# Kernel tuning notes

Measured on AMD Instinct MI355X. Metric: run time of the kernel, lower is better.

Reference implementation:

```python
import jax, jax.numpy as jnp
import numpy as np

H = 16            # num heads (sharded)
NOPE = 128        # qk_nope_head_dim
ROPE = 64         # qk_rope_head_dim
VD = 128          # v_head_dim
KV_RANK = 512
HEAD = NOPE + ROPE  # 192
SCALE = HEAD ** (-0.5)  # mscale == 1 (no yarn scaling)
EPS = 1e-6


def rmsnorm(x, w):
    var = jnp.mean(x * x, axis=-1, keepdims=True)
    return x * jax.lax.rsqrt(var + EPS) * w


def apply_rope(pe, cos, sin):
    # pe: [T, h, ROPE]; torch code de-interleaves pairs then applies
    # non-interleaved (rotate-half) rope: out = [e*cos - o*sin, o*cos + e*sin]
    e = pe[..., 0::2]
    o = pe[..., 1::2]
    c = cos[:, None, :]
    s = sin[:, None, :]
    return jnp.concatenate([e * c - o * s, o * c + e * s], axis=-1)


def setup_inputs() -> dict:
    key = jax.random.key(0)
    ks = jax.random.split(key, 10)
    T, D = 4096, 2048
    w = 0.02
    return {
        "hidden_states": jax.random.normal(ks[0], (T, D), jnp.float32),
        "cos": jax.random.uniform(ks[1], (T, ROPE // 2), jnp.float32),
        "sin": jax.random.uniform(ks[2], (T, ROPE // 2), jnp.float32),
        "w_q_a": jax.random.normal(ks[3], (D, 1536), jnp.float32) * w,
        "q_a_ln_w": jnp.ones((1536,), jnp.float32),
        "w_q_b": jax.random.normal(ks[4], (1536, H * HEAD), jnp.float32) * w,
        "w_kv_a": jax.random.normal(ks[5], (D, KV_RANK + ROPE), jnp.float32) * w,
        "kv_a_ln_w": jnp.ones((KV_RANK,), jnp.float32),
        "w_kv_b": jax.random.normal(ks[6], (KV_RANK, H * (NOPE + VD)), jnp.float32) * w,
        "w_o": jax.random.normal(ks[7], (H * VD, D), jnp.float32) * w,
        "batch_size": 2,
    }


def reference(hidden_states, cos, sin, w_q_a, q_a_ln_w, w_q_b, w_kv_a,
              kv_a_ln_w, w_kv_b, w_o, batch_size):
    T, D = hidden_states.shape
    B = int(batch_size)
    S = T // B

    # Q: low-rank down proj -> RMSNorm -> up proj
    q = rmsnorm(hidden_states @ w_q_a, q_a_ln_w) @ w_q_b
    q = q.reshape(T, H, HEAD)
    q_nope = q[..., :NOPE]
    q_pe = apply_rope(q[..., NOPE:], cos, sin)

    # KV: joint down proj with shared rope part (MQA-style)
    ckv = hidden_states @ w_kv_a                        # [T, 512+64]
    compressed_kv = ckv[:, :KV_RANK]
    k_pe = apply_rope(ckv[:, KV_RANK:][:, None, :], cos, sin)  # [T, 1, 64]
    kv = (rmsnorm(compressed_kv, kv_a_ln_w) @ w_kv_b).reshape(T, H, NOPE + VD)
    k_nope = kv[..., :NOPE]
    v = kv[..., NOPE:]                                   # [T, H, 128]

    # Assemble full query/key heads (value pad to 192 + final slice is a no-op
    # mathematically since padded dims are zero; we keep value dim = 128).
    query = jnp.concatenate([q_nope, q_pe], axis=-1)     # [T, H, 192]
    key = jnp.concatenate([k_nope, jnp.broadcast_to(k_pe, (T, H, ROPE))], axis=-1)

    # Causal (prefill) attention per sequence
    qb = query.reshape(B, S, H, HEAD)
    kb = key.reshape(B, S, H, HEAD)
    vb = v.reshape(B, S, H, VD)
    scores = jnp.einsum("bqhd,bkhd->bhqk", qb, kb) * SCALE
    causal = jnp.tril(jnp.ones((S, S), bool))
    scores = jnp.where(causal, scores, jnp.finfo(scores.dtype).min)
    probs = jax.nn.softmax(scores, axis=-1)
    attn = jnp.einsum("bhqk,bkhd->bqhd", probs, vb)      # [B, S, H, 128]

    return attn.reshape(T, H * VD) @ w_o
```

## Files before the change

kernel.cpp:

```cpp
#include <hip/hip_runtime.h>
#include <cstdint>
#include <cstddef>

#define TT 4096
#define DD 2048
#define NH 16
#define HEADD 192
#define NOPE 128
#define VDIM 128
#define SEQ 2048

typedef __bf16 bf16x8 __attribute__((ext_vector_type(8)));
typedef float f32x4 __attribute__((ext_vector_type(4)));
typedef unsigned int u32;

__device__ __forceinline__ float bf2f(unsigned short u) {
    union { unsigned int i; float f; } v; v.i = ((unsigned int)u) << 16; return v.f;
}
__device__ __forceinline__ unsigned short f2bf(float f) {
    union { float f; unsigned int i; } v; v.f = f;
    unsigned int r = v.i + 0x7FFFu + ((v.i >> 16) & 1u);
    return (unsigned short)(r >> 16);
}
__device__ __forceinline__ u32 pack2bf(float a, float b) {
    return (u32)f2bf(a) | ((u32)f2bf(b) << 16);
}
__device__ __forceinline__ void gload16(const unsigned short* g, unsigned short* l) {
    __builtin_amdgcn_global_load_lds((const __attribute__((address_space(1))) u32*)g,
                                     (__attribute__((address_space(3))) u32*)l, 16, 0, 0);
}

__global__ __launch_bounds__(256) void cvt_bf16_k(const float* __restrict__ x,
                                                  unsigned short* __restrict__ y, int n) {
    int i = (blockIdx.x * 256 + threadIdx.x) * 4;
    if (i < n) {
        float4 v = *(const float4*)(x + i);
        uint2 o;
        o.x = pack2bf(v.x, v.y);
        o.y = pack2bf(v.z, v.w);
        *(uint2*)(y + i) = o;
    }
}

__global__ __launch_bounds__(256) void transpose_cvt_k(const float* __restrict__ W,
                                                       unsigned short* __restrict__ Wt,
                                                       int K, int N) {
    __shared__ float tile[32][33];
    int n0 = blockIdx.x * 32, k0 = blockIdx.y * 32;
    int t = threadIdx.x, lr = t >> 5, lc = t & 31;
#pragma unroll
    for (int p = 0; p < 4; p++) {
        int k = k0 + lr + p * 8, n = n0 + lc;
        tile[lr + p * 8][lc] = (k < K && n < N) ? W[(size_t)k * N + n] : 0.f;
    }
    __syncthreads();
#pragma unroll
    for (int p = 0; p < 4; p++) {
        int n = n0 + lr + p * 8, k = k0 + lc;
        if (n < N && k < K) Wt[(size_t)n * K + k] = f2bf(tile[lc][lr + p * 8]);
    }
}

__global__ __launch_bounds__(256) void gemm_bf16_k(const unsigned short* __restrict__ A,
                                                   const unsigned short* __restrict__ Bt,
                                                   float* __restrict__ C,
                                                   int M, int N, int K) {
    __shared__ __align__(16) unsigned short As[128 * 32];
    __shared__ __align__(16) unsigned short Bs[128 * 32];
    int bm = blockIdx.y * 128, bn = blockIdx.x * 128;
    int t = threadIdx.x;
    int wave = t >> 6, lane = t & 63;
    int wr = (wave >> 1) * 64, wc = (wave & 1) * 64;
    int l15 = lane & 15, quad = lane >> 4;
    f32x4 acc[4][4];
    f32x4 zero = {0.f, 0.f, 0.f, 0.f};
#pragma unroll
    for (int i = 0; i < 4; i++)
#pragma unroll
        for (int j = 0; j < 4; j++) acc[i][j] = zero;
    int r0 = 16 * (2 * wave) + (lane >> 2);
    int cOff = (lane & 3) * 8;
    const unsigned short* gA0 = A + (size_t)(bm + r0) * K + cOff;
    const unsigned short* gA1 = A + (size_t)(bm + r0 + 16) * K + cOff;
    const unsigned short* gB0 = Bt + (size_t)(bn + r0) * K + cOff;
    const unsigned short* gB1 = Bt + (size_t)(bn + r0 + 16) * K + cOff;
    unsigned short* lA0 = &As[(2 * wave) * 512];
    unsigned short* lA1 = &As[(2 * wave + 1) * 512];
    unsigned short* lB0 = &Bs[(2 * wave) * 512];
    unsigned short* lB1 = &Bs[(2 * wave + 1) * 512];
    for (int k0 = 0; k0 < K; k0 += 32) {
        gload16(gA0 + k0, lA0);
        gload16(gA1 + k0, lA1);
        gload16(gB0 + k0, lB0);
        gload16(gB1 + k0, lB1);
        __syncthreads();
        bf16x8 af[4], bfr[4];
#pragma unroll
        for (int i = 0; i < 4; i++)
            af[i] = *(const bf16x8*)&As[(wr + i * 16 + l15) * 32 + quad * 8];
#pragma unroll
        for (int j = 0; j < 4; j++)
            bfr[j] = *(const bf16x8*)&Bs[(wc + j * 16 + l15) * 32 + quad * 8];
#pragma unroll
        for (int i = 0; i < 4; i++)
#pragma unroll
            for (int j = 0; j < 4; j++)
                acc[i][j] = __builtin_amdgcn_mfma_f32_16x16x32_bf16(af[i], bfr[j], acc[i][j], 0, 0, 0);
        __syncthreads();
    }
#pragma unroll
    for (int i = 0; i < 4; i++) {
        int row = bm + wr + i * 16 + quad * 4;
#pragma unroll
        for (int j = 0; j < 4; j++) {
            int col = bn + wc + j * 16 + l15;
            if (col < N) {
                float* cp = C + (size_t)row * N + col;
#pragma unroll
                for (int r = 0; r < 4; r++) cp[(size_t)r * N] = acc[i][j][r];
            }
        }
    }
}

__global__ __launch_bounds__(256) void gemm_bf16o_k(const unsigned short* __restrict__ A,
                                                    const unsigned short* __restrict__ Bt,
                                                    unsigned short* __restrict__ C,
                                                    int M, int N, int K) {
    __shared__ __align__(16) unsigned short As[128 * 32];
    __shared__ __align__(16) unsigned short Bs[128 * 32];
    int bm = blockIdx.y * 128, bn = blockIdx.x * 128;
    int t = threadIdx.x;
    int wave = t >> 6, lane = t & 63;
    int wr = (wave >> 1) * 64, wc = (wave & 1) * 64;
    int l15 = lane & 15, quad = lane >> 4;
    f32x4 acc[4][4];
    f32x4 zero = {0.f, 0.f, 0.f, 0.f};
#pragma unroll
    for (int i = 0; i < 4; i++)
#pragma unroll
        for (int j = 0; j < 4; j++) acc[i][j] = zero;
    int r0 = 16 * (2 * wave) + (lane >> 2);
    int cOff = (lane & 3) * 8;
    const unsigned short* gA0 = A + (size_t)(bm + r0) * K + cOff;
    const unsigned short* gA1 = A + (size_t)(bm + r0 + 16) * K + cOff;
    const unsigned short* gB0 = Bt + (size_t)(bn + r0) * K + cOff;
    const unsigned short* gB1 = Bt + (size_t)(bn + r0 + 16) * K + cOff;
    unsigned short* lA0 = &As[(2 * wave) * 512];
    unsigned short* lA1 = &As[(2 * wave + 1) * 512];
    unsigned short* lB0 = &Bs[(2 * wave) * 512];
    unsigned short* lB1 = &Bs[(2 * wave + 1) * 512];
    for (int k0 = 0; k0 < K; k0 += 32) {
        gload16(gA0 + k0, lA0);
        gload16(gA1 + k0, lA1);
        gload16(gB0 + k0, lB0);
        gload16(gB1 + k0, lB1);
        __syncthreads();
        bf16x8 af[4], bfr[4];
#pragma unroll
        for (int i = 0; i < 4; i++)
            af[i] = *(const bf16x8*)&As[(wr + i * 16 + l15) * 32 + quad * 8];
#pragma unroll
        for (int j = 0; j < 4; j++)
            bfr[j] = *(const bf16x8*)&Bs[(wc + j * 16 + l15) * 32 + quad * 8];
#pragma unroll
        for (int i = 0; i < 4; i++)
#pragma unroll
            for (int j = 0; j < 4; j++)
                acc[i][j] = __builtin_amdgcn_mfma_f32_16x16x32_bf16(af[i], bfr[j], acc[i][j], 0, 0, 0);
        __syncthreads();
    }
#pragma unroll
    for (int i = 0; i < 4; i++) {
        int row = bm + wr + i * 16 + quad * 4;
#pragma unroll
        for (int j = 0; j < 4; j++) {
            int col = bn + wc + j * 16 + l15;
            if (col < N) {
                unsigned short* cp = C + (size_t)row * N + col;
#pragma unroll
                for (int r = 0; r < 4; r++) cp[(size_t)r * N] = f2bf(acc[i][j][r]);
            }
        }
    }
}

#define KS_STRIDE 200
#define VT_STRIDE 72
#define CS_STRIDE 132

__global__ __launch_bounds__(256) void gemm_kv_k(const unsigned short* __restrict__ A,
                                                 const unsigned short* __restrict__ Bt,
                                                 unsigned short* __restrict__ Kb2,
                                                 unsigned short* __restrict__ Vt2) {
    const int K = 512;
    __shared__ __align__(16) unsigned short smem[128 * CS_STRIDE];
    unsigned short* As = smem;
    unsigned short* Bs = smem + 128 * 32;
    unsigned short* Cs = smem;
    int bm = blockIdx.y * 128, bn = blockIdx.x * 128;
    int t = threadIdx.x;
    int wave = t >> 6, lane = t & 63;
    int wr = (wave >> 1) * 64, wc = (wave & 1) * 64;
    int l15 = lane & 15, quad = lane >> 4;
    f32x4 acc[4][4];
    f32x4 zero = {0.f, 0.f, 0.f, 0.f};
#pragma unroll
    for (int i = 0; i < 4; i++)
#pragma unroll
        for (int j = 0; j < 4; j++) acc[i][j] = zero;
    int r0 = 16 * (2 * wave) + (lane >> 2);
    int cOff = (lane & 3) * 8;
    const unsigned short* gA0 = A + (size_t)(bm + r0) * K + cOff;
    const unsigned short* gA1 = A + (size_t)(bm + r0 + 16) * K + cOff;
    const unsigned short* gB0 = Bt + (size_t)(bn + r0) * K + cOff;
    const unsigned short* gB1 = Bt + (size_t)(bn + r0 + 16) * K + cOff;
    unsigned short* lA0 = &As[(2 * wave) * 512];
    unsigned short* lA1 = &As[(2 * wave + 1) * 512];
    unsigned short* lB0 = &Bs[(2 * wave) * 512];
    unsigned short* lB1 = &Bs[(2 * wave + 1) * 512];
    for (int k0 = 0; k0 < K; k0 += 32) {
        gload16(gA0 + k0, lA0);
        gload16(gA1 + k0, lA1);
        gload16(gB0 + k0, lB0);
        gload16(gB1 + k0, lB1);
        __syncthreads();
        bf16x8 af[4], bfr[4];
#pragma unroll
        for (int i = 0; i < 4; i++)
            af[i] = *(const bf16x8*)&As[(wr + i * 16 + l15) * 32 + quad * 8];
#pragma unroll
        for (int j = 0; j < 4; j++)
            bfr[j] = *(const bf16x8*)&Bs[(wc + j * 16 + l15) * 32 + quad * 8];
#pragma unroll
        for (int i = 0; i < 4; i++)
#pragma unroll
            for (int j = 0; j < 4; j++)
                acc[i][j] = __builtin_amdgcn_mfma_f32_16x16x32_bf16(af[i], bfr[j], acc[i][j], 0, 0, 0);
        __syncthreads();
    }
#pragma unroll
    for (int i = 0; i < 4; i++) {
        int lr = wr + i * 16 + quad * 4;
#pragma unroll
        for (int j = 0; j < 4; j++) {
            int lc = wc + j * 16 + l15;
#pragma unroll
            for (int r = 0; r < 4; r++)
                Cs[(lr + r) * CS_STRIDE + lc] = f2bf(acc[i][j][r]);
        }
    }
    __syncthreads();
    int hh = bn >> 8;
    bool isV = (bn & 255) != 0;
    if (!isV) {
        int row = t >> 1, halfc = t & 1;
        int gs = bm + row;
        int b2 = gs >> 11, s2 = gs & 2047;
        unsigned short* dp = Kb2 +
            ((size_t)((b2 * NH + hh) * 32 + (s2 >> 6)) * 64 + (s2 & 63)) * KS_STRIDE + halfc * 64;
        const unsigned short* sp = &Cs[row * CS_STRIDE + halfc * 64];
#pragma unroll
        for (int g = 0; g < 8; g++)
            *(uint4*)(dp + g * 8) = *(const uint4*)(sp + g * 8);
    } else {
        int kth = t >> 7, dim = t & 127;
        int gs0 = bm + kth * 64;
        int b2 = gs0 >> 11, s20 = gs0 & 2047;
        unsigned short* dp = Vt2 +
            ((size_t)((b2 * NH + hh) * 32 + (s20 >> 6)) * 128 + dim) * VT_STRIDE;
#pragma unroll
        for (int g = 0; g < 8; g++) {
            uint4 o;
            unsigned short* op = (unsigned short*)&o;
#pragma unroll
            for (int q2 = 0; q2 < 8; q2++)
                op[q2] = Cs[(kth * 64 + g * 8 + q2) * CS_STRIDE + dim];
            *(uint4*)(dp + g * 8) = o;
        }
    }
}

__global__ __launch_bounds__(256) void kpe_fill_k(const unsigned short* __restrict__ kpe,
                                                  unsigned short* __restrict__ Kb2) {
    int trow = blockIdx.x, t = threadIdx.x;
    int b = trow >> 11, s = trow & 2047;
    int kt = s >> 6, sr = s & 63;
    const unsigned short* src = kpe + trow * 64;
#pragma unroll
    for (int i = t; i < NH * 64; i += 256) {
        int h = i >> 6, d = i & 63;
        Kb2[(((size_t)(b * NH + h) * 32 + kt) * 64 + sr) * KS_STRIDE + 128 + d] = src[d];
    }
}

__global__ __launch_bounds__(256) void rmsnorm_bf_k(const unsigned short* __restrict__ x,
                                                    const float* __restrict__ w,
                                                    unsigned short* __restrict__ y) {
    int row = blockIdx.x, t = threadIdx.x;
    const unsigned short* xr = x + (size_t)row * 2112;
    float s = 0.f;
    for (int i = t; i < 1536; i += 256) { float v = bf2f(xr[i]); s += v * v; }
    __shared__ float red[256];
    red[t] = s; __syncthreads();
    for (int o = 128; o > 0; o >>= 1) { if (t < o) red[t] += red[t + o]; __syncthreads(); }
    float scale = rsqrtf(red[0] / 1536.f + 1e-6f);
    unsigned short* yr = y + (size_t)row * 1536;
    for (int i = t; i < 1536; i += 256) yr[i] = f2bf(bf2f(xr[i]) * scale * w[i]);
}

__global__ __launch_bounds__(256) void kvprep_bf_k(const unsigned short* __restrict__ qab,
                                                   const float* __restrict__ w,
                                                   const float* __restrict__ cosb,
                                                   const float* __restrict__ sinb,
                                                   unsigned short* __restrict__ ckvn,
                                                   unsigned short* __restrict__ kpe) {
    int row = blockIdx.x, t = threadIdx.x;
    const unsigned short* xr = qab + (size_t)row * 2112 + 1536;
    float s = 0.f;
#pragma unroll
    for (int i = t; i < 512; i += 256) { float v = bf2f(xr[i]); s += v * v; }
    __shared__ float red[256];
    red[t] = s; __syncthreads();
    for (int o = 128; o > 0; o >>= 1) { if (t < o) red[t] += red[t + o]; __syncthreads(); }
    float scale = rsqrtf(red[0] / 512.f + 1e-6f);
    unsigned short* yr = ckvn + (size_t)row * 512;
#pragma unroll
    for (int i = t; i < 512; i += 256) yr[i] = f2bf(bf2f(xr[i]) * scale * w[i]);
    if (t < 32) {
        float e = bf2f(xr[512 + 2 * t]), o = bf2f(xr[512 + 2 * t + 1]);
        float c = cosb[row * 32 + t], sn = sinb[row * 32 + t];
        kpe[row * 64 + t]      = f2bf(e * c - o * sn);
        kpe[row * 64 + 32 + t] = f2bf(o * c + e * sn);
    }
}

__global__ __launch_bounds__(256) void qprep_bf_k(const unsigned short* __restrict__ q,
                                                  const float* __restrict__ cosb,
                                                  const float* __restrict__ sinb,
                                                  unsigned short* __restrict__ Qb) {
    const float SCALE = 0.07216878364870323f;
    int trow = blockIdx.x, t = threadIdx.x;
    const unsigned short* qr = q + (size_t)trow * (NH * HEADD);
    unsigned short* yr = Qb + (size_t)trow * (NH * HEADD);
    for (int i = t; i < NH * HEADD; i += 256) {
        int h = i / HEADD, d = i - h * HEADD;
        float val;
        if (d < NOPE) val = bf2f(qr[i]);
        else {
            int j = d - NOPE;
            int jj = j & 31;
            const unsigned short* pe = qr + h * HEADD + NOPE;
            float e = bf2f(pe[2 * jj]), o = bf2f(pe[2 * jj + 1]);
            float c = cosb[trow * 32 + jj], sn = sinb[trow * 32 + jj];
            val = (j < 32) ? (e * c - o * sn) : (o * c + e * sn);
        }
        yr[i] = f2bf(val * SCALE);
    }
}

__global__ __launch_bounds__(512) void attn_mfma_k(const unsigned short* __restrict__ Qb,
                                                   const unsigned short* __restrict__ Kb2,
                                                   const unsigned short* __restrict__ Vt2,
                                                   unsigned short* __restrict__ Opart,
                                                   float* __restrict__ Mbuf,
                                                   float* __restrict__ Lbuf) {
    __shared__ __align__(16) unsigned short Ks[64 * KS_STRIDE];
    __shared__ __align__(16) unsigned short Vts[128 * VT_STRIDE];
    int xe = 39 - blockIdx.x;
    int h  = blockIdx.y;
    int b  = blockIdx.z;
    int qt = 0, accn = 0;
    while (true) { int c = (qt >> 2) + 1; if (xe < accn + c) break; accn += c; qt++; }
    int chunk = xe - accn;
    int t = threadIdx.x;
    int w = t >> 6, lane = t & 63;
    int l15 = lane & 15, quad = lane >> 4;
    int bh = b * NH + h;
    int q0 = b * SEQ + qt * 128;
    int qglob = qt * 128 + w * 16 + l15;
    int flat = bh * 40 + xe;

    bf16x8 qf[6];
    {
        const unsigned short* qbase = Qb + ((size_t)(q0 + w * 16 + l15) * NH + h) * HEADD + quad * 8;
#pragma unroll
        for (int c = 0; c < 6; c++)
            qf[c] = *(const bf16x8*)(qbase + c * 32);
    }
    f32x4 acc_o[8];
    f32x4 zero = {0.f, 0.f, 0.f, 0.f};
#pragma unroll
    for (int j = 0; j < 8; j++) acc_o[j] = zero;
    float mrun = -1e30f, lrun = 0.f;

    int kt0 = chunk * 8, kt1 = min(kt0 + 7, 2 * qt + 1);
    int cbeg = w * 5 + min(w, 3), cnt = (w < 3) ? 6 : 5;
    for (int kt = kt0; kt <= kt1; kt++) {
        __syncthreads();
        {
            const unsigned short* kg = Kb2 + ((size_t)bh * 32 + kt) * (64 * KS_STRIDE) + lane * 8;
            const unsigned short* vg = Vt2 + ((size_t)bh * 32 + kt) * (128 * VT_STRIDE) + lane * 8;
            for (int c = cbeg; c < cbeg + cnt; c++) {
                if (c < 25) gload16(kg + c * 512, &Ks[c * 512]);
                else        gload16(vg + (c - 25) * 512, &Vts[(c - 25) * 512]);
            }
        }
        __syncthreads();
        f32x4 acc_s[4];
#pragma unroll
        for (int j = 0; j < 4; j++) acc_s[j] = zero;
#pragma unroll
        for (int c = 0; c < 6; c++) {
#pragma unroll
            for (int j = 0; j < 4; j++) {
                bf16x8 kf = *(const bf16x8*)&Ks[(j * 16 + l15) * KS_STRIDE + c * 32 + quad * 8];
                acc_s[j] = __builtin_amdgcn_mfma_f32_16x16x32_bf16(kf, qf[c], acc_s[j], 0, 0, 0);
            }
        }
        float sv[4][4];
        const bool needmask = (kt * 64 + 63) > (qt * 128 + w * 16);
        if (needmask) {
#pragma unroll
            for (int j = 0; j < 4; j++) {
                int kbase = kt * 64 + j * 16 + quad * 4;
#pragma unroll
                for (int r = 0; r < 4; r++)
                    sv[j][r] = (kbase + r > qglob) ? -1e30f : acc_s[j][r];
            }
        } else {
#pragma unroll
            for (int j = 0; j < 4; j++)
#pragma unroll
                for (int r = 0; r < 4; r++) sv[j][r] = acc_s[j][r];
        }
        float v = sv[0][0];
#pragma unroll
        for (int j = 0; j < 4; j++)
#pragma unroll
            for (int r = 0; r < 4; r++) v = fmaxf(v, sv[j][r]);
        v = fmaxf(v, __shfl_xor(v, 16));
        v = fmaxf(v, __shfl_xor(v, 32));
        if (!__all(v - mrun <= 8.f)) {
            float mnew = fmaxf(mrun, v);
            float alpha = __expf(mrun - mnew);
            mrun = mnew;
            lrun *= alpha;
#pragma unroll
            for (int jt = 0; jt < 8; jt++)
#pragma unroll
                for (int r = 0; r < 4; r++) acc_o[jt][r] *= alpha;
        }
        float rs = 0.f;
#pragma unroll
        for (int j = 0; j < 4; j++)
#pragma unroll
            for (int r = 0; r < 4; r++) { float p = __expf(sv[j][r] - mrun); sv[j][r] = p; rs += p; }
        rs += __shfl_xor(rs, 16);
        rs += __shfl_xor(rs, 32);
        lrun += rs;
        u32 pk[4][2];
#pragma unroll
        for (int j = 0; j < 4; j++) {
            pk[j][0] = pack2bf(sv[j][0], sv[j][1]);
            pk[j][1] = pack2bf(sv[j][2], sv[j][3]);
        }
        int laneA = (((2 * quad) & 3) << 4) + l15;
        int laneB = (((2 * quad + 1) & 3) << 4) + l15;
        bool hi = (quad & 2) != 0;
#pragma unroll
        for (int c2 = 0; c2 < 2; c2++) {
            u32 a0 = __shfl(pk[2 * c2][0], laneA),     a1 = __shfl(pk[2 * c2][1], laneA);
            u32 b0 = __shfl(pk[2 * c2 + 1][0], laneA), b1 = __shfl(pk[2 * c2 + 1][1], laneA);
            u32 a2 = __shfl(pk[2 * c2][0], laneB),     a3 = __shfl(pk[2 * c2][1], laneB);
            u32 b2 = __shfl(pk[2 * c2 + 1][0], laneB), b3 = __shfl(pk[2 * c2 + 1][1], laneB);
            union { u32 d[4]; bf16x8 v8; } pf;
            pf.d[0] = hi ? b0 : a0;
            pf.d[1] = hi ? b1 : a1;
            pf.d[2] = hi ? b2 : a2;
            pf.d[3] = hi ? b3 : a3;
#pragma unroll
            for (int jt = 0; jt < 8; jt++) {
                bf16x8 vf = *(const bf16x8*)&Vts[(jt * 16 + l15) * VT_STRIDE + c2 * 32 + quad * 8];
                acc_o[jt] = __builtin_amdgcn_mfma_f32_16x16x32_bf16(vf, pf.v8, acc_o[jt], 0, 0, 0);
            }
        }
    }
    {
        int row = w * 16 + l15;
        unsigned short* op = Opart + (size_t)flat * 16384 + row * 128;
#pragma unroll
        for (int jt = 0; jt < 8; jt++) {
            uint2 o;
            o.x = pack2bf(acc_o[jt][0], acc_o[jt][1]);
            o.y = pack2bf(acc_o[jt][2], acc_o[jt][3]);
            *(uint2*)(op + jt * 16 + quad * 4) = o;
        }
        if (quad == 0) {
            Mbuf[(size_t)flat * 128 + row] = mrun;
            Lbuf[(size_t)flat * 128 + row] = lrun;
        }
    }
}

__global__ __launch_bounds__(256) void attn_combine_k(const unsigned short* __restrict__ Opart,
                                                      const float* __restrict__ Mbuf,
                                                      const float* __restrict__ Lbuf,
                                                      unsigned short* __restrict__ attnb) {
    int q64 = blockIdx.x, h = blockIdx.y, b = blockIdx.z;
    int qt = q64 >> 1, half = q64 & 1;
    int nch = (qt >> 2) + 1;
    int F = 0;
    for (int q = 0; q < qt; q++) F += (q >> 2) + 1;
    int flat0 = (b * NH + h) * 40 + F;
    int t = threadIdx.x;
    int row = t >> 2, d0 = (t & 3) * 32;
    int row128 = half * 64 + row;
    float mc[4], lc[4], wgt[4];
    float mstar = -1e30f;
#pragma unroll
    for (int c = 0; c < 4; c++) {
        if (c < nch) {
            mc[c] = Mbuf[(size_t)(flat0 + c) * 128 + row128];
            lc[c] = Lbuf[(size_t)(flat0 + c) * 128 + row128];
        } else { mc[c] = -1e30f; lc[c] = 0.f; }
        mstar = fmaxf(mstar, mc[c]);
    }
    float L = 0.f;
#pragma unroll
    for (int c = 0; c < 4; c++) { wgt[c] = __expf(mc[c] - mstar); L += wgt[c] * lc[c]; }
    float invL = 1.f / L;
    float acc[32];
#pragma unroll
    for (int j = 0; j < 32; j++) acc[j] = 0.f;
#pragma unroll
    for (int c = 0; c < 4; c++) {
        if (c < nch) {
            const unsigned short* src = Opart + (size_t)(flat0 + c) * 16384 + row128 * 128 + d0;
            float wc = wgt[c];
#pragma unroll
            for (int g = 0; g < 4; g++) {
                uint4 u = *(const uint4*)(src + g * 8);
                const unsigned short* sp = (const unsigned short*)&u;
#pragma unroll
                for (int j = 0; j < 8; j++) acc[g * 8 + j] += wc * bf2f(sp[j]);
            }
        }
    }
    unsigned short* dst = attnb + (size_t)(b * SEQ + q64 * 64 + row) * 2048 + h * 128 + d0;
#pragma unroll
    for (int g = 0; g < 4; g++) {
        uint4 o;
        unsigned short* sp = (unsigned short*)&o;
#pragma unroll
        for (int j = 0; j < 8; j++) sp[j] = f2bf(acc[g * 8 + j] * invL);
        *(uint4*)(dst + g * 8) = o;
    }
}

extern "C" void kernel_launch(void* const* d_in, const int* in_sizes, int n_in,
                              void* d_out, int out_size, void* d_ws, size_t ws_size,
                              hipStream_t stream) {
    const float* hs     = (const float*)d_in[0];
    const float* cosb   = (const float*)d_in[1];
    const float* sinb   = (const float*)d_in[2];
    const float* w_q_a  = (const float*)d_in[3];
    const float* q_ln   = (const float*)d_in[4];
    const float* w_q_b  = (const float*)d_in[5];
    const float* w_kv_a = (const float*)d_in[6];
    const float* kv_ln  = (const float*)d_in[7];
    const float* w_kv_b = (const float*)d_in[8];
    const float* w_o    = (const float*)d_in[9];
    float* out = (float*)d_out;

    char* base = (char*)d_ws;
    size_t off = 0;
    auto take = [&](size_t bytes) { void* p = base + off; off += (bytes + 255) & ~(size_t)255; return p; };
    unsigned short* wqabT = (unsigned short*)take((size_t)2112 * 2048 * 2);
    unsigned short* wqbT  = (unsigned short*)take((size_t)3072 * 1536 * 2);
    unsigned short* wkvbT = (unsigned short*)take((size_t)4096 * 512 * 2);
    unsigned short* woT   = (unsigned short*)take((size_t)2048 * 2048 * 2);
    unsigned short* hsb   = (unsigned short*)take((size_t)TT * DD * 2);
    unsigned short* qab   = (unsigned short*)take((size_t)TT * 2112 * 2);
    unsigned short* qan   = (unsigned short*)take((size_t)TT * 1536 * 2);
    unsigned short* ckvn  = (unsigned short*)take((size_t)TT * 512 * 2);
    unsigned short* kpe   = (unsigned short*)take((size_t)TT * 64 * 2);
    unsigned short* qb3   = (unsigned short*)take((size_t)TT * 3072 * 2);
    unsigned short* Qbuf  = (unsigned short*)take((size_t)TT * NH * HEADD * 2);
    unsigned short* Kb2   = (unsigned short*)take((size_t)32 * 32 * 64 * KS_STRIDE * 2);
    unsigned short* Vt2   = (unsigned short*)take((size_t)32 * 32 * 128 * VT_STRIDE * 2);
    unsigned short* attnb = (unsigned short*)take((size_t)TT * 2048 * 2);
    unsigned short* Opart = (unsigned short*)take((size_t)1280 * 16384 * 2);
    float* Mbuf = (float*)take((size_t)1280 * 128 * 4);
    float* Lbuf = (float*)take((size_t)1280 * 128 * 4);

    cvt_bf16_k<<<(TT * DD) / 1024, 256, 0, stream>>>(hs, hsb, TT * DD);
    transpose_cvt_k<<<dim3(1536 / 32, 2048 / 32), 256, 0, stream>>>(w_q_a, wqabT, 2048, 1536);
    transpose_cvt_k<<<dim3(18, 2048 / 32), 256, 0, stream>>>(w_kv_a, wqabT + (size_t)1536 * 2048, 2048, 576);
    transpose_cvt_k<<<dim3(3072 / 32, 1536 / 32), 256, 0, stream>>>(w_q_b, wqbT, 1536, 3072);
    transpose_cvt_k<<<dim3(4096 / 32, 512 / 32), 256, 0, stream>>>(w_kv_b, wkvbT, 512, 4096);
    transpose_cvt_k<<<dim3(2048 / 32, 2048 / 32), 256, 0, stream>>>(w_o, woT, 2048, 2048);

    gemm_bf16o_k<<<dim3(17, 32), 256, 0, stream>>>(hsb, wqabT, qab, 4096, 2112, 2048);
    rmsnorm_bf_k<<<4096, 256, 0, stream>>>(qab, q_ln, qan);
    kvprep_bf_k<<<4096, 256, 0, stream>>>(qab, kv_ln, cosb, sinb, ckvn, kpe);
    gemm_bf16o_k<<<dim3(24, 32), 256, 0, stream>>>(qan, wqbT, qb3, 4096, 3072, 1536);
    qprep_bf_k<<<4096, 256, 0, stream>>>(qb3, cosb, sinb, Qbuf);
    gemm_kv_k<<<dim3(32, 32), 256, 0, stream>>>(ckvn, wkvbT, Kb2, Vt2);
    kpe_fill_k<<<4096, 256, 0, stream>>>(kpe, Kb2);
    attn_mfma_k<<<dim3(40, 16, 2), 512, 0, stream>>>(Qbuf, Kb2, Vt2, Opart, Mbuf, Lbuf);
    attn_combine_k<<<dim3(32, 16, 2), 256, 0, stream>>>(Opart, Mbuf, Lbuf, attnb);
    gemm_bf16_k<<<dim3(16, 32), 256, 0, stream>>>(attnb, woT, out, 4096, 2048, 2048);
}
```

Baseline: 527.4 us.

## Add double-buffered 512-thread GEMM with swizzled LDS for projection matmuls

Adds a templated 512-thread GEMM kernel with 128xBN tiles, a K-step of 64, double-buffered LDS with prefetch of the next tile interleaved with MFMA compute, XOR-swizzled shared-memory layout to avoid bank conflicts, and s_setprio around MFMA bursts. It replaces the q_a/kv_a, q_b and output projection GEMMs; the 64-column remainder of the first GEMM is handled by the old kernel, which gains an ldc parameter. The aim is to hide global-load latency and improve data reuse, at the cost of more LDS per block and lower occupancy.

After: 514.1 us. 2.5% less time.

```diff
diff --git a/kernel.cpp b/kernel.cpp
--- a/kernel.cpp
+++ b/kernel.cpp
@@ -61,10 +61,124 @@
     }
 }
 
-__global__ __launch_bounds__(256) void gemm_bf16_k(const unsigned short* __restrict__ A,
-                                                   const unsigned short* __restrict__ Bt,
-                                                   float* __restrict__ C,
-                                                   int M, int N, int K) {
+#define GMFMA __builtin_amdgcn_mfma_f32_16x16x32_bf16
+
+template <int BN, typename OT>
+__global__ __launch_bounds__(512) void gemm256_k(const unsigned short* __restrict__ A,
+                                                 const unsigned short* __restrict__ Bt,
+                                                 OT* __restrict__ C,
+                                                 int M, int N, int K) {
+    constexpr int NREP = BN / 64;
+    constexpr int NB = BN / 64;
+    constexpr int TILE_E = 8192 + BN * 64;
+    __shared__ __align__(16) unsigned short lds[2 * TILE_E];
+    const int t = threadIdx.x;
+    const int w = t >> 6, lane = t & 63;
+    const int wr = w >> 2, wc = w & 3;
+    const int l15 = lane & 15, quad = lane >> 4;
+    const int bm = blockIdx.y * 128, bn = blockIdx.x * BN;
+    const int srow = w * 8 + (lane >> 3);
+    const int scol = 8 * ((lane & 7) ^ (lane >> 3));
+    const unsigned short* Ag = A + (size_t)(bm + srow) * K + scol;
+    const unsigned short* Bg = Bt + (size_t)(bn + srow) * K + scol;
+    const int rc0 = (quad * 8) ^ ((l15 & 7) * 8);
+    const int rc1 = (32 + quad * 8) ^ ((l15 & 7) * 8);
+    f32x4 acc[4][NREP];
+    f32x4 zero = {0.f, 0.f, 0.f, 0.f};
+#pragma unroll
+    for (int i = 0; i < 4; i++)
+#pragma unroll
+        for (int n = 0; n < NREP; n++) acc[i][n] = zero;
+    const int NT = K >> 6;
+#pragma unroll
+    for (int c = 0; c < 2; c++)
+        gload16(Ag + (size_t)c * 64 * K, &lds[c * 4096 + w * 512]);
+#pragma unroll
+    for (int c = 0; c < NB; c++)
+        gload16(Bg + (size_t)c * 64 * K, &lds[8192 + c * 4096 + w * 512]);
+
+    for (int kt = 0; kt < NT; kt++) {
+        const int cb = (kt & 1) * TILE_E;
+        const int nb = TILE_E - cb;
+        const bool more = (kt + 1) < NT;
+        asm volatile("s_waitcnt vmcnt(0)" ::: "memory");
+        __builtin_amdgcn_s_barrier();
+        asm volatile("" ::: "memory");
+        const unsigned short* Agk = Ag + (size_t)(kt + 1) * 64;
+        const unsigned short* Bgk = Bg + (size_t)(kt + 1) * 64;
+        if (more) {
+            gload16(Agk, &lds[nb + w * 512]);
+            gload16(Agk + (size_t)64 * K, &lds[nb + 4096 + w * 512]);
+#pragma unroll
+            for (int c = 0; c < NB / 2; c++)
+                gload16(Bgk + (size_t)c * 64 * K, &lds[nb + 8192 + c * 4096 + w * 512]);
+        }
+        bf16x8 a0[2][2], b[NREP][2];
+#pragma unroll
+        for (int j = 0; j < 2; j++) {
+            int rl = wr * 64 + j * 16 + l15;
+            a0[j][0] = *(const bf16x8*)&lds[cb + rl * 64 + rc0];
+            a0[j][1] = *(const bf16x8*)&lds[cb + rl * 64 + rc1];
+        }
+#pragma unroll
+        for (int n = 0; n < NREP; n++) {
+            int rl = wc * (BN / 4) + n * 16 + l15;
+            b[n][0] = *(const bf16x8*)&lds[cb + 8192 + rl * 64 + rc0];
+            b[n][1] = *(const bf16x8*)&lds[cb + 8192 + rl * 64 + rc1];
+        }
+        __builtin_amdgcn_s_setprio(1);
+#pragma unroll
+        for (int j = 0; j < 2; j++)
+#pragma unroll
+            for (int n = 0; n < NREP; n++) {
+                acc[j][n] = GMFMA(a0[j][0], b[n][0], acc[j][n], 0, 0, 0);
+                acc[j][n] = GMFMA(a0[j][1], b[n][1], acc[j][n], 0, 0, 0);
+            }
+        __builtin_amdgcn_s_setprio(0);
+        __builtin_amdgcn_s_barrier();
+        if (more) {
+#pragma unroll
+            for (int c = NB / 2; c < NB; c++)
+                gload16(Bgk + (size_t)c * 64 * K, &lds[nb + 8192 + c * 4096 + w * 512]);
+        }
+        bf16x8 a1[2][2];
+#pragma unroll
+        for (int j = 0; j < 2; j++) {
+            int rl = wr * 64 + 32 + j * 16 + l15;
+            a1[j][0] = *(const bf16x8*)&lds[cb + rl * 64 + rc0];
+            a1[j][1] = *(const bf16x8*)&lds[cb + rl * 64 + rc1];
+        }
+        __builtin_amdgcn_s_setprio(1);
+#pragma unroll
+        for (int j = 0; j < 2; j++)
+#pragma unroll
+            for (int n = 0; n < NREP; n++) {
+                acc[2 + j][n] = GMFMA(a1[j][0], b[n][0], acc[2 + j][n], 0, 0, 0);
+                acc[2 + j][n] = GMFMA(a1[j][1], b[n][1], acc[2 + j][n], 0, 0, 0);
+            }
+        __builtin_amdgcn_s_setprio(0);
+    }
+#pragma unroll
+    for (int mi = 0; mi < 4; mi++) {
+        int row = bm + wr * 64 + mi * 16 + quad * 4;
+#pragma unroll
+        for (int n = 0; n < NREP; n++) {
+            int col = bn + wc * (BN / 4) + n * 16 + l15;
+            OT* cp = C + (size_t)row * N + col;
+#pragma unroll
+            for (int r = 0; r < 4; r++) {
+                float v = acc[mi][n][r];
+                if constexpr (sizeof(OT) == 2) cp[(size_t)r * N] = f2bf(v);
+                else                            cp[(size_t)r * N] = v;
+            }
+        }
+    }
+}
+
+__global__ __launch_bounds__(256) void gemm_bf16o_k(const unsigned short* __restrict__ A,
+                                                    const unsigned short* __restrict__ Bt,
+                                                    unsigned short* __restrict__ C,
+                                                    int M, int N, int K, int ldc) {
     __shared__ __align__(16) unsigned short As[128 * 32];
     __shared__ __align__(16) unsigned short Bs[128 * 32];
     int bm = blockIdx.y * 128, bn = blockIdx.x * 128;
@@ -105,7 +219,7 @@
         for (int i = 0; i < 4; i++)
 #pragma unroll
             for (int j = 0; j < 4; j++)
-                acc[i][j] = __builtin_amdgcn_mfma_f32_16x16x32_bf16(af[i], bfr[j], acc[i][j], 0, 0, 0);
+                acc[i][j] = GMFMA(af[i], bfr[j], acc[i][j], 0, 0, 0);
         __syncthreads();
     }
 #pragma unroll
@@ -115,20 +229,27 @@
         for (int j = 0; j < 4; j++) {
             int col = bn + wc + j * 16 + l15;
             if (col < N) {
-                float* cp = C + (size_t)row * N + col;
-#pragma unroll
-                for (int r = 0; r < 4; r++) cp[(size_t)r * N] = acc[i][j][r];
-            }
-        }
-    }
-}
-
-__global__ __launch_bounds__(256) void gemm_bf16o_k(const unsigned short* __restrict__ A,
-                                                    const unsigned short* __restrict__ Bt,
-                                                    unsigned short* __restrict__ C,
-                                                    int M, int N, int K) {
-    __shared__ __align__(16) unsigned short As[128 * 32];
-    __shared__ __align__(16) unsigned short Bs[128 * 32];
+                unsigned short* cp = C + (size_t)row * ldc + col;
+#pragma unroll
+                for (int r = 0; r < 4; r++) cp[(size_t)r * ldc] = f2bf(acc[i][j][r]);
+            }
+        }
+    }
+}
+
+#define KS_STRIDE 200
+#define VT_STRIDE 72
+#define CS_STRIDE 132
+
+__global__ __launch_bounds__(256) void gemm_kv_k(const unsigned short* __restrict__ A,
+                                                 const unsigned short* __restrict__ Bt,
+                                                 unsigned short* __restrict__ Kb2,
+                                                 unsigned short* __restrict__ Vt2) {
+    const int K = 512;
+    __shared__ __align__(16) unsigned short smem[128 * CS_STRIDE];
+    unsigned short* As = smem;
+    unsigned short* Bs = smem + 128 * 32;
+    unsigned short* Cs = smem;
     int bm = blockIdx.y * 128, bn = blockIdx.x * 128;
     int t = threadIdx.x;
     int wave = t >> 6, lane = t & 63;
@@ -167,76 +288,7 @@
         for (int i = 0; i < 4; i++)
 #pragma unroll
             for (int j = 0; j < 4; j++)
-                acc[i][j] = __builtin_amdgcn_mfma_f32_16x16x32_bf16(af[i], bfr[j], acc[i][j], 0, 0, 0);
-        __syncthreads();
-    }
-#pragma unroll
-    for (int i = 0; i < 4; i++) {
-        int row = bm + wr + i * 16 + quad * 4;
-#pragma unroll
-        for (int j = 0; j < 4; j++) {
-            int col = bn + wc + j * 16 + l15;
-            if (col < N) {
-                unsigned short* cp = C + (size_t)row * N + col;
-#pragma unroll
-                for (int r = 0; r < 4; r++) cp[(size_t)r * N] = f2bf(acc[i][j][r]);
-            }
-        }
-    }
-}
-
-#define KS_STRIDE 200
-#define VT_STRIDE 72
-#define CS_STRIDE 132
-
-__global__ __launch_bounds__(256) void gemm_kv_k(const unsigned short* __restrict__ A,
-                                                 const unsigned short* __restrict__ Bt,
-                                                 unsigned short* __restrict__ Kb2,
-                                                 unsigned short* __restrict__ Vt2) {
-    const int K = 512;
-    __shared__ __align__(16) unsigned short smem[128 * CS_STRIDE];
-    unsigned short* As = smem;
-    unsigned short* Bs = smem + 128 * 32;
-    unsigned short* Cs = smem;
-    int bm = blockIdx.y * 128, bn = blockIdx.x * 128;
-    int t = threadIdx.x;
-    int wave = t >> 6, lane = t & 63;
-    int wr = (wave >> 1) * 64, wc = (wave & 1) * 64;
-    int l15 = lane & 15, quad = lane >> 4;
-    f32x4 acc[4][4];
-    f32x4 zero = {0.f, 0.f, 0.f, 0.f};
-#pragma unroll
-    for (int i = 0; i < 4; i++)
-#pragma unroll
-        for (int j = 0; j < 4; j++) acc[i][j] = zero;
-    int r0 = 16 * (2 * wave) + (lane >> 2);
-    int cOff = (lane & 3) * 8;
-    const unsigned short* gA0 = A + (size_t)(bm + r0) * K + cOff;
-    const unsigned short* gA1 = A + (size_t)(bm + r0 + 16) * K + cOff;
-    const unsigned short* gB0 = Bt + (size_t)(bn + r0) * K + cOff;
-    const unsigned short* gB1 = Bt + (size_t)(bn + r0 + 16) * K + cOff;
-    unsigned short* lA0 = &As[(2 * wave) * 512];
-    unsigned short* lA1 = &As[(2 * wave + 1) * 512];
-    unsigned short* lB0 = &Bs[(2 * wave) * 512];
-    unsigned short* lB1 = &Bs[(2 * wave + 1) * 512];
-    for (int k0 = 0; k0 < K; k0 += 32) {
-        gload16(gA0 + k0, lA0);
-        gload16(gA1 + k0, lA1);
-        gload16(gB0 + k0, lB0);
-        gload16(gB1 + k0, lB1);
-        __syncthreads();
-        bf16x8 af[4], bfr[4];
-#pragma unroll
-        for (int i = 0; i < 4; i++)
-            af[i] = *(const bf16x8*)&As[(wr + i * 16 + l15) * 32 + quad * 8];
-#pragma unroll
-        for (int j = 0; j < 4; j++)
-            bfr[j] = *(const bf16x8*)&Bs[(wc + j * 16 + l15) * 32 + quad * 8];
-#pragma unroll
-        for (int i = 0; i < 4; i++)
-#pragma unroll
-            for (int j = 0; j < 4; j++)
-                acc[i][j] = __builtin_amdgcn_mfma_f32_16x16x32_bf16(af[i], bfr[j], acc[i][j], 0, 0, 0);
+                acc[i][j] = GMFMA(af[i], bfr[j], acc[i][j], 0, 0, 0);
         __syncthreads();
     }
 #pragma unroll
@@ -415,7 +467,7 @@
 #pragma unroll
             for (int j = 0; j < 4; j++) {
                 bf16x8 kf = *(const bf16x8*)&Ks[(j * 16 + l15) * KS_STRIDE + c * 32 + quad * 8];
-                acc_s[j] = __builtin_amdgcn_mfma_f32_16x16x32_bf16(kf, qf[c], acc_s[j], 0, 0, 0);
+                acc_s[j] = GMFMA(kf, qf[c], acc_s[j], 0, 0, 0);
             }
         }
         float sv[4][4];
@@ -482,7 +534,7 @@
 #pragma unroll
             for (int jt = 0; jt < 8; jt++) {
                 bf16x8 vf = *(const bf16x8*)&Vts[(jt * 16 + l15) * VT_STRIDE + c2 * 32 + quad * 8];
-                acc_o[jt] = __builtin_amdgcn_mfma_f32_16x16x32_bf16(vf, pf.v8, acc_o[jt], 0, 0, 0);
+                acc_o[jt] = GMFMA(vf, pf.v8, acc_o[jt], 0, 0, 0);
             }
         }
     }
@@ -601,14 +653,16 @@
     transpose_cvt_k<<<dim3(4096 / 32, 512 / 32), 256, 0, stream>>>(w_kv_b, wkvbT, 512, 4096);
     transpose_cvt_k<<<dim3(2048 / 32, 2048 / 32), 256, 0, stream>>>(w_o, woT, 2048, 2048);
 
-    gemm_bf16o_k<<<dim3(17, 32), 256, 0, stream>>>(hsb, wqabT, qab, 4096, 2112, 2048);
+    gemm256_k<256, unsigned short><<<dim3(8, 32), 512, 0, stream>>>(hsb, wqabT, qab, 4096, 2112, 2048);
+    gemm_bf16o_k<<<dim3(1, 32), 256, 0, stream>>>(hsb, wqabT + (size_t)2048 * 2048, qab + 2048,
+                                                  4096, 64, 2048, 2112);
     rmsnorm_bf_k<<<4096, 256, 0, stream>>>(qab, q_ln, qan);
     kvprep_bf_k<<<4096, 256, 0, stream>>>(qab, kv_ln, cosb, sinb, ckvn, kpe);
-    gemm_bf16o_k<<<dim3(24, 32), 256, 0, stream>>>(qan, wqbT, qb3, 4096, 3072, 1536);
+    gemm256_k<192, unsigned short><<<dim3(16, 32), 512, 0, stream>>>(qan, wqbT, qb3, 4096, 3072, 1536);
     qprep_bf_k<<<4096, 256, 0, stream>>>(qb3, cosb, sinb, Qbuf);
     gemm_kv_k<<<dim3(32, 32), 256, 0, stream>>>(ckvn, wkvbT, Kb2, Vt2);
     kpe_fill_k<<<4096, 256, 0, stream>>>(kpe, Kb2);
     attn_mfma_k<<<dim3(40, 16, 2), 512, 0, stream>>>(Qbuf, Kb2, Vt2, Opart, Mbuf, Lbuf);
     attn_combine_k<<<dim3(32, 16, 2), 256, 0, stream>>>(Opart, Mbuf, Lbuf, attnb);
-    gemm_bf16_k<<<dim3(16, 32), 256, 0, stream>>>(attnb, woT, out, 4096, 2048, 2048);
-}
+    gemm256_k<256, float><<<dim3(8, 32), 512, 0, stream>>>(attnb, woT, out, 4096, 2048, 2048);
+}
```
